# Optimization experiments

Measured on AMD Instinct MI355X. Metric: run time of the kernel, lower is better.

The kernel has to match this reference:

```python
import jax, jax.numpy as jnp
import numpy as np

B, D = 2048, 1024
TEMP = 0.1
LAMBDA_CS_REG = 0.5


def setup_inputs() -> dict:
    key = jax.random.key(0)
    k1, k2, k3, k4, k5 = jax.random.split(key, 5)
    return {
        "english": jax.random.normal(k1, (B, D), dtype=jnp.float32),
        "etok": jax.random.normal(k2, (B, D), dtype=jnp.float32),
        "ktoe": jax.random.normal(k3, (B, D), dtype=jnp.float32),
        "korean": jax.random.normal(k4, (B, D), dtype=jnp.float32),
        "cs_ratios": jax.random.uniform(k5, (B,), dtype=jnp.float32),
    }


def _l2norm(x):
    return x / jnp.linalg.norm(x, axis=1, keepdims=True)


def reference(english, etok, ktoe, korean, cs_ratios):
    e = _l2norm(english)   # [B,D]
    et = _l2norm(etok)
    kt = _l2norm(ktoe)
    k = _l2norm(korean)
    bsz = e.shape[0]

    # Stack the 4 embedding types: order [english, korean, etok, ktoe]
    embs = jnp.stack([e, k, et, kt])           # [4,B,D]

    # Similarities of each anchor row i against every row j of every type t.
    S_e = jnp.einsum("bd,tnd->tbn", e, embs) / TEMP   # [4,B,B] english anchors
    S_k = jnp.einsum("bd,tnd->tbn", k, embs) / TEMP   # [4,B,B] korean anchors
    exp_Se = jnp.exp(S_e)
    exp_Sk = jnp.exp(S_k)

    diag_e = jnp.diagonal(exp_Se, axis1=1, axis2=2)   # [4,B] exp(sim(anchor_i, type_i))
    diag_k = jnp.diagonal(exp_Sk, axis1=1, axis2=2)

    # Negatives: all 4 types for every j != i.
    neg_e = exp_Se.sum(axis=(0, 2)) - diag_e.sum(axis=0)   # [B]
    neg_k = exp_Sk.sum(axis=(0, 2)) - diag_k.sum(axis=0)

    # Positives: eng anchor -> {etok_i, ktoe_i, korean_i}; kor anchor -> {etok_i, ktoe_i, english_i}
    num_e = diag_e[1] + diag_e[2] + diag_e[3]
    num_k = diag_k[0] + diag_k[2] + diag_k[3]

    loss_e = -jnp.log(num_e / (num_e + neg_e))
    loss_k = -jnp.log(num_k / (num_k + neg_k))
    contrastive_loss = (loss_e + loss_k).sum() / (2 * bsz)

    # Code-switch regularization
    r = cs_ratios[:, None]                              # [B,1]
    etok_reg = jnp.linalg.norm(et - (r * e + (1 - r) * k), axis=1)
    ktoe_reg = jnp.linalg.norm(kt - ((1 - r) * e + r * k), axis=1)
    cs_reg_loss = (etok_reg + ktoe_reg).sum() / bsz

    total_loss = contrastive_loss + LAMBDA_CS_REG * cs_reg_loss
    return total_loss, contrastive_loss, cs_reg_loss
```

## Files before the change

kernel.cpp:

```cpp
#include <hip/hip_runtime.h>
#include <hip/hip_bf16.h>
#include <math.h>

#define NB   2048
#define ND   1024
#define INV_TEMP 10.0f
#define LAMBDA_CS 0.5f

using short8  = __attribute__((ext_vector_type(8))) short;
using floatx4 = __attribute__((ext_vector_type(4))) float;

__device__ __forceinline__ ushort f32_to_bf16_rne(float f) {
  union { float f; unsigned u; } v; v.f = f;
  unsigned u = v.u;
  u += 0x7FFFu + ((u >> 16) & 1u);
  return (ushort)(u >> 16);
}

__global__ __launch_bounds__(256) void k_norm_reg(
    const float* __restrict__ e, const float* __restrict__ k,
    const float* __restrict__ et, const float* __restrict__ kt,
    const float* __restrict__ ratios,
    ushort* __restrict__ M, float* __restrict__ reg_partial)
{
  const int b = blockIdx.x, tid = threadIdx.x;
  const int wave = tid >> 6, lane = tid & 63;

  float4 ve  = ((const float4*)(e  + (size_t)b * ND))[tid];
  float4 vk  = ((const float4*)(k  + (size_t)b * ND))[tid];
  float4 vet = ((const float4*)(et + (size_t)b * ND))[tid];
  float4 vkt = ((const float4*)(kt + (size_t)b * ND))[tid];

  float s0 = ve.x*ve.x + ve.y*ve.y + ve.z*ve.z + ve.w*ve.w;
  float s1 = vk.x*vk.x + vk.y*vk.y + vk.z*vk.z + vk.w*vk.w;
  float s2 = vet.x*vet.x + vet.y*vet.y + vet.z*vet.z + vet.w*vet.w;
  float s3 = vkt.x*vkt.x + vkt.y*vkt.y + vkt.z*vkt.z + vkt.w*vkt.w;
  #pragma unroll
  for (int o = 1; o < 64; o <<= 1) {
    s0 += __shfl_xor(s0, o); s1 += __shfl_xor(s1, o);
    s2 += __shfl_xor(s2, o); s3 += __shfl_xor(s3, o);
  }
  __shared__ float red[4][4];
  if (lane == 0) { red[wave][0] = s0; red[wave][1] = s1; red[wave][2] = s2; red[wave][3] = s3; }
  __syncthreads();
  const float ie  = 1.0f / sqrtf(red[0][0] + red[1][0] + red[2][0] + red[3][0]);
  const float ik  = 1.0f / sqrtf(red[0][1] + red[1][1] + red[2][1] + red[3][1]);
  const float iet = 1.0f / sqrtf(red[0][2] + red[1][2] + red[2][2] + red[3][2]);
  const float ikt = 1.0f / sqrtf(red[0][3] + red[1][3] + red[2][3] + red[3][3]);

  {
    ushort o4[4];
    o4[0] = f32_to_bf16_rne(ve.x * ie);  o4[1] = f32_to_bf16_rne(ve.y * ie);
    o4[2] = f32_to_bf16_rne(ve.z * ie);  o4[3] = f32_to_bf16_rne(ve.w * ie);
    *(ushort4*)(M + ((size_t)0 * NB + b) * ND + tid * 4) = *(ushort4*)o4;
    o4[0] = f32_to_bf16_rne(vk.x * ik);  o4[1] = f32_to_bf16_rne(vk.y * ik);
    o4[2] = f32_to_bf16_rne(vk.z * ik);  o4[3] = f32_to_bf16_rne(vk.w * ik);
    *(ushort4*)(M + ((size_t)1 * NB + b) * ND + tid * 4) = *(ushort4*)o4;
    o4[0] = f32_to_bf16_rne(vet.x * iet); o4[1] = f32_to_bf16_rne(vet.y * iet);
    o4[2] = f32_to_bf16_rne(vet.z * iet); o4[3] = f32_to_bf16_rne(vet.w * iet);
    *(ushort4*)(M + ((size_t)2 * NB + b) * ND + tid * 4) = *(ushort4*)o4;
    o4[0] = f32_to_bf16_rne(vkt.x * ikt); o4[1] = f32_to_bf16_rne(vkt.y * ikt);
    o4[2] = f32_to_bf16_rne(vkt.z * ikt); o4[3] = f32_to_bf16_rne(vkt.w * ikt);
    *(ushort4*)(M + ((size_t)3 * NB + b) * ND + tid * 4) = *(ushort4*)o4;
  }

  const float r = ratios[b], rm = 1.0f - r;
  float a1 = 0.f, a2 = 0.f;
  {
    float en, kn, d1, d2;
    en = ve.x*ie; kn = vk.x*ik;
    d1 = vet.x*iet - (r*en + rm*kn); d2 = vkt.x*ikt - (rm*en + r*kn);
    a1 += d1*d1; a2 += d2*d2;
    en = ve.y*ie; kn = vk.y*ik;
    d1 = vet.y*iet - (r*en + rm*kn); d2 = vkt.y*ikt - (rm*en + r*kn);
    a1 += d1*d1; a2 += d2*d2;
    en = ve.z*ie; kn = vk.z*ik;
    d1 = vet.z*iet - (r*en + rm*kn); d2 = vkt.z*ikt - (rm*en + r*kn);
    a1 += d1*d1; a2 += d2*d2;
    en = ve.w*ie; kn = vk.w*ik;
    d1 = vet.w*iet - (r*en + rm*kn); d2 = vkt.w*ikt - (rm*en + r*kn);
    a1 += d1*d1; a2 += d2*d2;
  }
  #pragma unroll
  for (int o = 1; o < 64; o <<= 1) { a1 += __shfl_xor(a1, o); a2 += __shfl_xor(a2, o); }
  __shared__ float red2[4][2];
  if (lane == 0) { red2[wave][0] = a1; red2[wave][1] = a2; }
  __syncthreads();
  if (tid == 0) {
    float t1 = red2[0][0] + red2[1][0] + red2[2][0] + red2[3][0];
    float t2 = red2[0][1] + red2[1][1] + red2[2][1] + red2[3][1];
    reg_partial[b] = sqrtf(t1) + sqrtf(t2);
  }
}

__global__ __launch_bounds__(256) void k_gemm_exp_rowsum(
    const ushort* __restrict__ M,
    float* __restrict__ rsp,
    float* __restrict__ diag)
{
  __shared__ ushort As[128 * 32];
  __shared__ ushort Bs[128 * 32];
  __shared__ float redR[256];
  __shared__ float redC[256];

  int bx, by;
  {
    int idx = blockIdx.x;
    if (idx < 1024) { by = idx >> 5; bx = 32 + (idx & 31); }
    else {
      int t = idx - 1024; by = 0;
      while (t >= 32 - by) { t -= 32 - by; ++by; }
      bx = by + t;
    }
  }
  const bool sym = (bx < 32) && (bx > by);
  const int j0 = bx * 128;
  const int i0 = by * 128;

  const int tid  = threadIdx.x;
  const int wave = tid >> 6;
  const int lane = tid & 63;
  const int q = lane >> 4;
  const int m = lane & 15;
  const int wrow = (wave >> 1) * 64;
  const int wcol = (wave & 1) * 64;

  floatx4 acc[4][4] = {};

  const int srow = lane >> 2;
  const int scol = (lane & 3) ^ ((srow >> 1) & 3);
  const int c0 = wave * 2, c1 = c0 + 1;

  const ushort* gA = M + (size_t)i0 * ND;
  const ushort* gB = M + (size_t)j0 * ND;

  int aoff[4], boff[4];
  #pragma unroll
  for (int x = 0; x < 4; ++x) {
    const int sw = (q ^ ((m >> 1) & 3)) * 8;
    aoff[x] = (wrow + x * 16 + m) * 32 + sw;
    boff[x] = (wcol + x * 16 + m) * 32 + sw;
  }

  for (int k0 = 0; k0 < ND; k0 += 32) {
    __syncthreads();
    {
      const ushort* g = gA + (size_t)(c0 * 16 + srow) * ND + k0 + scol * 8;
      __builtin_amdgcn_global_load_lds(
          (const __attribute__((address_space(1))) unsigned int*)g,
          (__attribute__((address_space(3))) unsigned int*)&As[c0 * 512], 16, 0, 0);
    }
    {
      const ushort* g = gA + (size_t)(c1 * 16 + srow) * ND + k0 + scol * 8;
      __builtin_amdgcn_global_load_lds(
          (const __attribute__((address_space(1))) unsigned int*)g,
          (__attribute__((address_space(3))) unsigned int*)&As[c1 * 512], 16, 0, 0);
    }
    {
      const ushort* g = gB + (size_t)(c0 * 16 + srow) * ND + k0 + scol * 8;
      __builtin_amdgcn_global_load_lds(
          (const __attribute__((address_space(1))) unsigned int*)g,
          (__attribute__((address_space(3))) unsigned int*)&Bs[c0 * 512], 16, 0, 0);
    }
    {
      const ushort* g = gB + (size_t)(c1 * 16 + srow) * ND + k0 + scol * 8;
      __builtin_amdgcn_global_load_lds(
          (const __attribute__((address_space(1))) unsigned int*)g,
          (__attribute__((address_space(3))) unsigned int*)&Bs[c1 * 512], 16, 0, 0);
    }
    __syncthreads();

    short8 af[4], bf[4];
    #pragma unroll
    for (int x = 0; x < 4; ++x) {
      af[x] = *(const short8*)&As[aoff[x]];
      bf[x] = *(const short8*)&Bs[boff[x]];
    }
    #pragma unroll
    for (int mi = 0; mi < 4; ++mi)
      #pragma unroll
      for (int ni = 0; ni < 4; ++ni)
        acc[mi][ni] = __builtin_amdgcn_mfma_f32_16x16x32_bf16(
            af[mi], bf[ni], acc[mi][ni], 0, 0, 0);
  }

  float colAcc[4] = {0.f, 0.f, 0.f, 0.f};
  #pragma unroll
  for (int mi = 0; mi < 4; ++mi) {
    #pragma unroll
    for (int r = 0; r < 4; ++r) {
      const int ig = i0 + wrow + mi * 16 + q * 4 + r;
      float s = 0.f;
      #pragma unroll
      for (int ni = 0; ni < 4; ++ni) {
        float v = __expf(acc[mi][ni][r] * INV_TEMP);
        s += v;
        colAcc[ni] += v;
        const int jg = j0 + wcol + ni * 16 + m;
        if ((jg & (NB - 1)) == (ig & (NB - 1))) {
          diag[(((ig >> 11) << 2) + (jg >> 11)) * NB + (ig & (NB - 1))] = v;
        }
      }
      s += __shfl_xor(s, 1);
      s += __shfl_xor(s, 2);
      s += __shfl_xor(s, 4);
      s += __shfl_xor(s, 8);
      if (m == 0) redR[(wave & 1) * 128 + wrow + mi * 16 + q * 4 + r] = s;
    }
  }
  #pragma unroll
  for (int ni = 0; ni < 4; ++ni) {
    float c = colAcc[ni];
    c += __shfl_xor(c, 16);
    c += __shfl_xor(c, 32);
    if (q == 0) redC[(wave >> 1) * 128 + wcol + ni * 16 + m] = c;
  }
  __syncthreads();
  if (tid < 128) {
    rsp[(size_t)bx * 4096 + i0 + tid] = redR[tid] + redR[128 + tid];
    if (sym)
      rsp[(size_t)by * 4096 + j0 + tid] = redC[tid] + redC[128 + tid];
  }
}

__global__ __launch_bounds__(256) void k_rowloss(
    const float* __restrict__ rsp, const float* __restrict__ diag,
    float* __restrict__ loss_row)
{
  const int n = blockIdx.x * 256 + threadIdx.x;
  float se = 0.f, sk = 0.f;
  #pragma unroll 8
  for (int s = 0; s < 64; ++s) {
    se += rsp[s * 4096 + n];
    sk += rsp[s * 4096 + 2048 + n];
  }
  const float d_ee  = diag[0 * NB + n];
  const float d_ek  = diag[1 * NB + n];
  const float d_eet = diag[2 * NB + n];
  const float d_ekt = diag[3 * NB + n];
  const float d_kk  = diag[5 * NB + n];
  const float d_ket = diag[6 * NB + n];
  const float d_kkt = diag[7 * NB + n];
  const float num_e = d_ek + d_eet + d_ekt;
  const float den_e = se - d_ee;
  const float num_k = d_ek + d_ket + d_kkt;
  const float den_k = sk - d_kk;
  loss_row[n] = logf(den_e / num_e) + logf(den_k / num_k);
}

__global__ __launch_bounds__(256) void k_out(
    const float* __restrict__ loss_row, const float* __restrict__ reg_partial,
    float* __restrict__ out)
{
  const int tid = threadIdx.x;
  const int wave = tid >> 6, lane = tid & 63;
  float l = 0.f, g = 0.f;
  #pragma unroll
  for (int i = 0; i < 8; ++i) {
    l += loss_row[tid + i * 256];
    g += reg_partial[tid + i * 256];
  }
  #pragma unroll
  for (int o = 1; o < 64; o <<= 1) { l += __shfl_xor(l, o); g += __shfl_xor(g, o); }
  __shared__ float rl[4], rg[4];
  if (lane == 0) { rl[wave] = l; rg[wave] = g; }
  __syncthreads();
  if (tid == 0) {
    float contrastive = (rl[0] + rl[1] + rl[2] + rl[3]) * (1.0f / (2.0f * NB));
    float cs = (rg[0] + rg[1] + rg[2] + rg[3]) * (1.0f / NB);
    out[0] = contrastive + LAMBDA_CS * cs;
    out[1] = contrastive;
    out[2] = cs;
  }
}

extern "C" void kernel_launch(void* const* d_in, const int* in_sizes, int n_in,
                              void* d_out, int out_size, void* d_ws, size_t ws_size,
                              hipStream_t stream) {
  const float* english = (const float*)d_in[0];
  const float* etok    = (const float*)d_in[1];
  const float* ktoe    = (const float*)d_in[2];
  const float* korean  = (const float*)d_in[3];
  const float* ratios  = (const float*)d_in[4];

  char* ws = (char*)d_ws;
  const size_t OFF_M    = 0;
  const size_t OFF_RSP  = OFF_M + (size_t)8192 * 1024 * 2;
  const size_t OFF_DIAG = OFF_RSP + (size_t)64 * 4096 * 4;
  const size_t OFF_REG  = OFF_DIAG + 8 * NB * sizeof(float);
  const size_t OFF_LOSS = OFF_REG + NB * sizeof(float);

  ushort* M           = (ushort*)(ws + OFF_M);
  float* rsp          = (float*)(ws + OFF_RSP);
  float* diag         = (float*)(ws + OFF_DIAG);
  float* reg_partial  = (float*)(ws + OFF_REG);
  float* loss_row     = (float*)(ws + OFF_LOSS);

  k_norm_reg<<<dim3(NB), 256, 0, stream>>>(english, korean, etok, ktoe, ratios, M, reg_partial);
  k_gemm_exp_rowsum<<<dim3(1552), 256, 0, stream>>>(M, rsp, diag);
  k_rowloss<<<dim3(8), 256, 0, stream>>>(rsp, diag, loss_row);
  k_out<<<dim3(1), 256, 0, stream>>>(loss_row, reg_partial, (float*)d_out);
}
```

Before: 165.2 us.

## Use 256x256 double-buffered GEMM tiles with phased loads and fused final reduction

Rewrites the similarity GEMM to use 256x256 output tiles with 512 threads, double-buffered LDS with 64-wide K slices, and interleaved global-to-LDS staging across phases with explicit waitcnt/barrier and setprio around the MFMA bursts. This is meant to raise arithmetic intensity and hide load latency compared with the previous single-buffered 128x128 tiles. The row-loss and output kernels are merged into one 1024-thread kernel, removing one launch. The cost is higher register and LDS use (128KB of LDS, 32 accumulators per thread), fewer blocks (392) on the device, and a fragile hand-written pipeline schedule.

```diff
diff --git a/kernel.cpp b/kernel.cpp
--- a/kernel.cpp
+++ b/kernel.cpp
@@ -1,5 +1,4 @@
 #include <hip/hip_runtime.h>
-#include <hip/hip_bf16.h>
 #include <math.h>
 
 #define NB   2048
@@ -93,111 +92,141 @@
   }
 }
 
-__global__ __launch_bounds__(256) void k_gemm_exp_rowsum(
+
+#define STAGE_A(TT, HH, BUF) do {                                              \
+  _Pragma("unroll")                                                            \
+  for (int L_ = 0; L_ < 2; ++L_) {                                             \
+    const int u_ = L_ * 512 + tid;                                             \
+    const int rr_ = u_ >> 3;                                                   \
+    const int sc_ = ((u_ & 7) * 16) ^ ((rr_ & 7) << 4);                        \
+    const ushort* gp_ = M + (size_t)(i0 + (HH)*128 + rr_) * ND + (TT)*64 + (sc_ >> 1); \
+    __builtin_amdgcn_global_load_lds(                                          \
+        (const __attribute__((address_space(1))) unsigned int*)gp_,            \
+        (__attribute__((address_space(3))) unsigned int*)&As[BUF][(HH)*8192 + L_*4096 + wave*512], \
+        16, 0, 0);                                                             \
+  }                                                                            \
+} while (0)
+
+#define STAGE_B(TT, HH, BUF) do {                                              \
+  _Pragma("unroll")                                                            \
+  for (int L_ = 0; L_ < 2; ++L_) {                                             \
+    const int u_ = L_ * 512 + tid;                                             \
+    const int rr_ = u_ >> 3;                                                   \
+    const int sc_ = ((u_ & 7) * 16) ^ ((rr_ & 7) << 4);                        \
+    const ushort* gp_ = M + (size_t)(j0 + (HH)*128 + rr_) * ND + (TT)*64 + (sc_ >> 1); \
+    __builtin_amdgcn_global_load_lds(                                          \
+        (const __attribute__((address_space(1))) unsigned int*)gp_,            \
+        (__attribute__((address_space(3))) unsigned int*)&Bs[BUF][(HH)*8192 + L_*4096 + wave*512], \
+        16, 0, 0);                                                             \
+  }                                                                            \
+} while (0)
+
+#define PHASE(BUF, MQ, KK, LOADB, WAIT, STMT) do {                             \
+  short8 af_[4];                                                               \
+  _Pragma("unroll")                                                            \
+  for (int mi_ = 0; mi_ < 4; ++mi_) {                                          \
+    const int row_ = wrow + ((MQ)*4 + mi_)*16 + m;                             \
+    const int cb_ = ((KK)*64 + q*16) ^ ((row_ & 7) << 4);                      \
+    af_[mi_] = *(const short8*)&As[BUF][row_*64 + (cb_ >> 1)];                 \
+  }                                                                            \
+  if (LOADB) {                                                                 \
+    _Pragma("unroll")                                                          \
+    for (int ni_ = 0; ni_ < 4; ++ni_) {                                        \
+      const int rb_ = wcol + ni_*16 + m;                                       \
+      const int cb_ = ((KK)*64 + q*16) ^ ((rb_ & 7) << 4);                     \
+      bfr[KK][ni_] = *(const short8*)&Bs[BUF][rb_*64 + (cb_ >> 1)];            \
+    }                                                                          \
+  }                                                                            \
+  STMT;                                                                        \
+  __builtin_amdgcn_s_barrier();                                                \
+  asm volatile("s_waitcnt lgkmcnt(0)" ::: "memory");                           \
+  __builtin_amdgcn_s_setprio(1);                                               \
+  _Pragma("unroll")                                                            \
+  for (int mi_ = 0; mi_ < 4; ++mi_)                                            \
+    _Pragma("unroll")                                                          \
+    for (int ni_ = 0; ni_ < 4; ++ni_)                                          \
+      acc[(MQ)*4 + mi_][ni_] = __builtin_amdgcn_mfma_f32_16x16x32_bf16(        \
+          af_[mi_], bfr[KK][ni_], acc[(MQ)*4 + mi_][ni_], 0, 0, 0);            \
+  __builtin_amdgcn_s_setprio(0);                                               \
+  if (WAIT) asm volatile("s_waitcnt vmcnt(4)" ::: "memory");                   \
+  __builtin_amdgcn_s_barrier();                                                \
+} while (0)
+
+__global__ __launch_bounds__(512, 2) void k_gemm_exp_rowsum(
     const ushort* __restrict__ M,
     float* __restrict__ rsp,
     float* __restrict__ diag)
 {
-  __shared__ ushort As[128 * 32];
-  __shared__ ushort Bs[128 * 32];
-  __shared__ float redR[256];
-  __shared__ float redC[256];
+  __shared__ __align__(16) ushort As[2][16384];
+  __shared__ __align__(16) ushort Bs[2][16384];
 
   int bx, by;
   {
     int idx = blockIdx.x;
-    if (idx < 1024) { by = idx >> 5; bx = 32 + (idx & 31); }
+    if (idx < 256) { by = idx >> 4; bx = 16 + (idx & 15); }
     else {
-      int t = idx - 1024; by = 0;
-      while (t >= 32 - by) { t -= 32 - by; ++by; }
+      int t = idx - 256; by = 0;
+      while (t >= 16 - by) { t -= 16 - by; ++by; }
       bx = by + t;
     }
   }
-  const bool sym = (bx < 32) && (bx > by);
-  const int j0 = bx * 128;
-  const int i0 = by * 128;
+  const bool sym = (bx < 16) && (bx > by);
+  const int i0 = by * 256;
+  const int j0 = bx * 256;
 
   const int tid  = threadIdx.x;
   const int wave = tid >> 6;
   const int lane = tid & 63;
   const int q = lane >> 4;
   const int m = lane & 15;
-  const int wrow = (wave >> 1) * 64;
-  const int wcol = (wave & 1) * 64;
-
-  floatx4 acc[4][4] = {};
-
-  const int srow = lane >> 2;
-  const int scol = (lane & 3) ^ ((srow >> 1) & 3);
-  const int c0 = wave * 2, c1 = c0 + 1;
-
-  const ushort* gA = M + (size_t)i0 * ND;
-  const ushort* gB = M + (size_t)j0 * ND;
-
-  int aoff[4], boff[4];
-  #pragma unroll
-  for (int x = 0; x < 4; ++x) {
-    const int sw = (q ^ ((m >> 1) & 3)) * 8;
-    aoff[x] = (wrow + x * 16 + m) * 32 + sw;
-    boff[x] = (wcol + x * 16 + m) * 32 + sw;
-  }
-
-  for (int k0 = 0; k0 < ND; k0 += 32) {
-    __syncthreads();
-    {
-      const ushort* g = gA + (size_t)(c0 * 16 + srow) * ND + k0 + scol * 8;
-      __builtin_amdgcn_global_load_lds(
-          (const __attribute__((address_space(1))) unsigned int*)g,
-          (__attribute__((address_space(3))) unsigned int*)&As[c0 * 512], 16, 0, 0);
-    }
-    {
-      const ushort* g = gA + (size_t)(c1 * 16 + srow) * ND + k0 + scol * 8;
-      __builtin_amdgcn_global_load_lds(
-          (const __attribute__((address_space(1))) unsigned int*)g,
-          (__attribute__((address_space(3))) unsigned int*)&As[c1 * 512], 16, 0, 0);
-    }
-    {
-      const ushort* g = gB + (size_t)(c0 * 16 + srow) * ND + k0 + scol * 8;
-      __builtin_amdgcn_global_load_lds(
-          (const __attribute__((address_space(1))) unsigned int*)g,
-          (__attribute__((address_space(3))) unsigned int*)&Bs[c0 * 512], 16, 0, 0);
-    }
-    {
-      const ushort* g = gB + (size_t)(c1 * 16 + srow) * ND + k0 + scol * 8;
-      __builtin_amdgcn_global_load_lds(
-          (const __attribute__((address_space(1))) unsigned int*)g,
-          (__attribute__((address_space(3))) unsigned int*)&Bs[c1 * 512], 16, 0, 0);
-    }
-    __syncthreads();
-
-    short8 af[4], bf[4];
-    #pragma unroll
-    for (int x = 0; x < 4; ++x) {
-      af[x] = *(const short8*)&As[aoff[x]];
-      bf[x] = *(const short8*)&Bs[boff[x]];
-    }
-    #pragma unroll
-    for (int mi = 0; mi < 4; ++mi)
-      #pragma unroll
-      for (int ni = 0; ni < 4; ++ni)
-        acc[mi][ni] = __builtin_amdgcn_mfma_f32_16x16x32_bf16(
-            af[mi], bf[ni], acc[mi][ni], 0, 0, 0);
-  }
+  const int wr = wave >> 2;
+  const int wc = wave & 3;
+  const int wrow = wr * 128;
+  const int wcol = wc * 64;
+
+  floatx4 acc[8][4] = {};
+  short8 bfr[2][4];
+
+  STAGE_A(0, 0, 0); STAGE_A(0, 1, 0);
+  STAGE_B(0, 0, 0); STAGE_B(0, 1, 0);
+  STAGE_B(1, 0, 1); STAGE_B(1, 1, 1);
+  asm volatile("s_waitcnt vmcnt(4)" ::: "memory");
+  __builtin_amdgcn_s_barrier();
+
+  #pragma unroll 1
+  for (int i = 0; i < 8; ++i) {
+    const int t1 = 2*i + 1;
+    const int t2 = (2*i + 2) & 15;
+    const int t3 = (2*i + 3) & 15;
+    PHASE(0, 0, 0, 1, 0, STAGE_A(t1, 0, 1));
+    PHASE(0, 0, 1, 1, 0, STAGE_A(t1, 1, 1));
+    PHASE(0, 1, 0, 0, 0, STAGE_B(t2, 0, 0));
+    PHASE(0, 1, 1, 0, 1, STAGE_B(t2, 1, 0));
+    PHASE(1, 0, 0, 1, 0, STAGE_A(t2, 0, 0));
+    PHASE(1, 0, 1, 1, 0, STAGE_A(t2, 1, 0));
+    PHASE(1, 1, 0, 0, 0, STAGE_B(t3, 0, 1));
+    PHASE(1, 1, 1, 0, 1, STAGE_B(t3, 1, 1));
+  }
+
+  __syncthreads();
+
+  float* redR = (float*)&As[0][0];
+  float* redC = redR + 1024;
 
   float colAcc[4] = {0.f, 0.f, 0.f, 0.f};
   #pragma unroll
-  for (int mi = 0; mi < 4; ++mi) {
+  for (int mi = 0; mi < 8; ++mi) {
     #pragma unroll
     for (int r = 0; r < 4; ++r) {
       const int ig = i0 + wrow + mi * 16 + q * 4 + r;
       float s = 0.f;
       #pragma unroll
       for (int ni = 0; ni < 4; ++ni) {
-        float v = __expf(acc[mi][ni][r] * INV_TEMP);
+        const float v = __expf(acc[mi][ni][r] * INV_TEMP);
         s += v;
         colAcc[ni] += v;
         const int jg = j0 + wcol + ni * 16 + m;
-        if ((jg & (NB - 1)) == (ig & (NB - 1))) {
+        if (((ig ^ jg) & (NB - 1)) == 0) {
           diag[(((ig >> 11) << 2) + (jg >> 11)) * NB + (ig & (NB - 1))] = v;
         }
       }
@@ -205,7 +234,7 @@
       s += __shfl_xor(s, 2);
       s += __shfl_xor(s, 4);
       s += __shfl_xor(s, 8);
-      if (m == 0) redR[(wave & 1) * 128 + wrow + mi * 16 + q * 4 + r] = s;
+      if (m == 0) redR[wc * 256 + wrow + mi * 16 + q * 4 + r] = s;
     }
   }
   #pragma unroll
@@ -213,61 +242,58 @@
     float c = colAcc[ni];
     c += __shfl_xor(c, 16);
     c += __shfl_xor(c, 32);
-    if (q == 0) redC[(wave >> 1) * 128 + wcol + ni * 16 + m] = c;
-  }
-  __syncthreads();
-  if (tid < 128) {
-    rsp[(size_t)bx * 4096 + i0 + tid] = redR[tid] + redR[128 + tid];
-    if (sym)
-      rsp[(size_t)by * 4096 + j0 + tid] = redC[tid] + redC[128 + tid];
-  }
-}
-
-__global__ __launch_bounds__(256) void k_rowloss(
+    if (q == 0) redC[wr * 256 + wcol + ni * 16 + m] = c;
+  }
+  __syncthreads();
+  if (tid < 256) {
+    const float rs = redR[tid] + redR[256 + tid] + redR[512 + tid] + redR[768 + tid];
+    rsp[(size_t)bx * 4096 + i0 + tid] = rs;
+    if (sym) {
+      const float cs = redC[tid] + redC[256 + tid];
+      rsp[(size_t)by * 4096 + j0 + tid] = cs;
+    }
+  }
+}
+
+__global__ __launch_bounds__(1024) void k_final(
     const float* __restrict__ rsp, const float* __restrict__ diag,
-    float* __restrict__ loss_row)
-{
-  const int n = blockIdx.x * 256 + threadIdx.x;
-  float se = 0.f, sk = 0.f;
-  #pragma unroll 8
-  for (int s = 0; s < 64; ++s) {
-    se += rsp[s * 4096 + n];
-    sk += rsp[s * 4096 + 2048 + n];
-  }
-  const float d_ee  = diag[0 * NB + n];
-  const float d_ek  = diag[1 * NB + n];
-  const float d_eet = diag[2 * NB + n];
-  const float d_ekt = diag[3 * NB + n];
-  const float d_kk  = diag[5 * NB + n];
-  const float d_ket = diag[6 * NB + n];
-  const float d_kkt = diag[7 * NB + n];
-  const float num_e = d_ek + d_eet + d_ekt;
-  const float den_e = se - d_ee;
-  const float num_k = d_ek + d_ket + d_kkt;
-  const float den_k = sk - d_kk;
-  loss_row[n] = logf(den_e / num_e) + logf(den_k / num_k);
-}
-
-__global__ __launch_bounds__(256) void k_out(
-    const float* __restrict__ loss_row, const float* __restrict__ reg_partial,
-    float* __restrict__ out)
+    const float* __restrict__ reg_partial, float* __restrict__ out)
 {
   const int tid = threadIdx.x;
   const int wave = tid >> 6, lane = tid & 63;
   float l = 0.f, g = 0.f;
   #pragma unroll
-  for (int i = 0; i < 8; ++i) {
-    l += loss_row[tid + i * 256];
-    g += reg_partial[tid + i * 256];
+  for (int h = 0; h < 2; ++h) {
+    const int n = tid + h * 1024;
+    float se = 0.f, sk = 0.f;
+    #pragma unroll 8
+    for (int s = 0; s < 32; ++s) {
+      se += rsp[s * 4096 + n];
+      sk += rsp[s * 4096 + 2048 + n];
+    }
+    const float d_ee  = diag[0 * NB + n];
+    const float d_ek  = diag[1 * NB + n];
+    const float d_eet = diag[2 * NB + n];
+    const float d_ekt = diag[3 * NB + n];
+    const float d_kk  = diag[5 * NB + n];
+    const float d_ket = diag[6 * NB + n];
+    const float d_kkt = diag[7 * NB + n];
+    const float num_e = d_ek + d_eet + d_ekt;
+    const float num_k = d_ek + d_ket + d_kkt;
+    l += logf((se - d_ee) / num_e) + logf((sk - d_kk) / num_k);
+    g += reg_partial[n];
   }
   #pragma unroll
   for (int o = 1; o < 64; o <<= 1) { l += __shfl_xor(l, o); g += __shfl_xor(g, o); }
-  __shared__ float rl[4], rg[4];
+  __shared__ float rl[16], rg[16];
   if (lane == 0) { rl[wave] = l; rg[wave] = g; }
   __syncthreads();
   if (tid == 0) {
-    float contrastive = (rl[0] + rl[1] + rl[2] + rl[3]) * (1.0f / (2.0f * NB));
-    float cs = (rg[0] + rg[1] + rg[2] + rg[3]) * (1.0f / NB);
+    float L = 0.f, G = 0.f;
+    #pragma unroll
+    for (int i = 0; i < 16; ++i) { L += rl[i]; G += rg[i]; }
+    const float contrastive = L * (1.0f / (2.0f * NB));
+    const float cs = G * (1.0f / NB);
     out[0] = contrastive + LAMBDA_CS * cs;
     out[1] = contrastive;
     out[2] = cs;
@@ -286,18 +312,15 @@
   char* ws = (char*)d_ws;
   const size_t OFF_M    = 0;
   const size_t OFF_RSP  = OFF_M + (size_t)8192 * 1024 * 2;
-  const size_t OFF_DIAG = OFF_RSP + (size_t)64 * 4096 * 4;
+  const size_t OFF_DIAG = OFF_RSP + (size_t)32 * 4096 * 4;
   const size_t OFF_REG  = OFF_DIAG + 8 * NB * sizeof(float);
-  const size_t OFF_LOSS = OFF_REG + NB * sizeof(float);
 
   ushort* M           = (ushort*)(ws + OFF_M);
   float* rsp          = (float*)(ws + OFF_RSP);
   float* diag         = (float*)(ws + OFF_DIAG);
   float* reg_partial  = (float*)(ws + OFF_REG);
-  float* loss_row     = (float*)(ws + OFF_LOSS);
 
   k_norm_reg<<<dim3(NB), 256, 0, stream>>>(english, korean, etok, ktoe, ratios, M, reg_partial);
-  k_gemm_exp_rowsum<<<dim3(1552), 256, 0, stream>>>(M, rsp, diag);
-  k_rowloss<<<dim3(8), 256, 0, stream>>>(rsp, diag, loss_row);
-  k_out<<<dim3(1), 256, 0, stream>>>(loss_row, reg_partial, (float*)d_out);
-}
+  k_gemm_exp_rowsum<<<dim3(392), 512, 0, stream>>>(M, rsp, diag);
+  k_final<<<dim3(1), 1024, 0, stream>>>(rsp, diag, reg_partial, (float*)d_out);
+}
```

Result: slower. 171.9 us (+4.0%).

## Triple-buffer GEMM LDS loads and replace partial rowsum buffers with atomics

Applied to the files above, without the earlier changes.

The GEMM main loop now prefetches K-tiles two steps ahead into a three-stage LDS ring, using explicit vmcnt waits and a single barrier per step. This is meant to hide global-load latency behind the MFMA work, at the cost of three times the LDS per block. Row sums are now accumulated with atomicAdd into a single 4096-entry buffer that the norm kernel zeroes, replacing the 64-way partial array. The rowloss and output kernels are merged into one 1024-thread kernel, which removes one launch and the partial-sum traffic.

```diff
diff --git a/kernel.cpp b/kernel.cpp
--- a/kernel.cpp
+++ b/kernel.cpp
@@ -1,5 +1,4 @@
 #include <hip/hip_runtime.h>
-#include <hip/hip_bf16.h>
 #include <math.h>
 
 #define NB   2048
@@ -21,7 +20,8 @@
     const float* __restrict__ e, const float* __restrict__ k,
     const float* __restrict__ et, const float* __restrict__ kt,
     const float* __restrict__ ratios,
-    ushort* __restrict__ M, float* __restrict__ reg_partial)
+    ushort* __restrict__ M, float* __restrict__ reg_partial,
+    float* __restrict__ rowsum)
 {
   const int b = blockIdx.x, tid = threadIdx.x;
   const int wave = tid >> 6, lane = tid & 63;
@@ -90,16 +90,35 @@
     float t1 = red2[0][0] + red2[1][0] + red2[2][0] + red2[3][0];
     float t2 = red2[0][1] + red2[1][1] + red2[2][1] + red2[3][1];
     reg_partial[b] = sqrtf(t1) + sqrtf(t2);
-  }
-}
-
-__global__ __launch_bounds__(256) void k_gemm_exp_rowsum(
+    rowsum[b] = 0.f;
+    rowsum[NB + b] = 0.f;
+  }
+}
+
+
+#define GLDS(GP, LP)                                                           \
+  __builtin_amdgcn_global_load_lds(                                            \
+      (const __attribute__((address_space(1))) unsigned int*)(GP),             \
+      (__attribute__((address_space(3))) unsigned int*)(LP), 16, 0, 0)
+
+#define STAGE(TT, BUF) do {                                                    \
+  GLDS(gA + (size_t)(c0 * 16 + srow) * ND + (TT) * 32 + scol * 8,              \
+       &As[BUF][c0 * 512]);                                                    \
+  GLDS(gA + (size_t)(c1 * 16 + srow) * ND + (TT) * 32 + scol * 8,              \
+       &As[BUF][c1 * 512]);                                                    \
+  GLDS(gB + (size_t)(c0 * 16 + srow) * ND + (TT) * 32 + scol * 8,              \
+       &Bs[BUF][c0 * 512]);                                                    \
+  GLDS(gB + (size_t)(c1 * 16 + srow) * ND + (TT) * 32 + scol * 8,              \
+       &Bs[BUF][c1 * 512]);                                                    \
+} while (0)
+
+__global__ __launch_bounds__(256, 3) void k_gemm_exp_rowsum(
     const ushort* __restrict__ M,
-    float* __restrict__ rsp,
+    float* __restrict__ rowsum,
     float* __restrict__ diag)
 {
-  __shared__ ushort As[128 * 32];
-  __shared__ ushort Bs[128 * 32];
+  __shared__ __align__(16) ushort As[3][4096];
+  __shared__ __align__(16) ushort Bs[3][4096];
   __shared__ float redR[256];
   __shared__ float redC[256];
 
@@ -142,47 +161,41 @@
     boff[x] = (wcol + x * 16 + m) * 32 + sw;
   }
 
-  for (int k0 = 0; k0 < ND; k0 += 32) {
-    __syncthreads();
-    {
-      const ushort* g = gA + (size_t)(c0 * 16 + srow) * ND + k0 + scol * 8;
-      __builtin_amdgcn_global_load_lds(
-          (const __attribute__((address_space(1))) unsigned int*)g,
-          (__attribute__((address_space(3))) unsigned int*)&As[c0 * 512], 16, 0, 0);
-    }
-    {
-      const ushort* g = gA + (size_t)(c1 * 16 + srow) * ND + k0 + scol * 8;
-      __builtin_amdgcn_global_load_lds(
-          (const __attribute__((address_space(1))) unsigned int*)g,
-          (__attribute__((address_space(3))) unsigned int*)&As[c1 * 512], 16, 0, 0);
-    }
-    {
-      const ushort* g = gB + (size_t)(c0 * 16 + srow) * ND + k0 + scol * 8;
-      __builtin_amdgcn_global_load_lds(
-          (const __attribute__((address_space(1))) unsigned int*)g,
-          (__attribute__((address_space(3))) unsigned int*)&Bs[c0 * 512], 16, 0, 0);
-    }
-    {
-      const ushort* g = gB + (size_t)(c1 * 16 + srow) * ND + k0 + scol * 8;
-      __builtin_amdgcn_global_load_lds(
-          (const __attribute__((address_space(1))) unsigned int*)g,
-          (__attribute__((address_space(3))) unsigned int*)&Bs[c1 * 512], 16, 0, 0);
-    }
-    __syncthreads();
+  STAGE(0, 0);
+  STAGE(1, 1);
+  asm volatile("s_waitcnt vmcnt(4)" ::: "memory");
+  __builtin_amdgcn_s_barrier();
+
+  int bcur = 0, bnext = 1, bstage = 2;
+  #pragma unroll 1
+  for (int t = 0; t < 32; ++t) {
+    STAGE((t + 2) & 31, bstage);
 
     short8 af[4], bf[4];
     #pragma unroll
     for (int x = 0; x < 4; ++x) {
-      af[x] = *(const short8*)&As[aoff[x]];
-      bf[x] = *(const short8*)&Bs[boff[x]];
+      af[x] = *(const short8*)&As[bcur][aoff[x]];
+      bf[x] = *(const short8*)&Bs[bcur][boff[x]];
     }
+    asm volatile("s_waitcnt lgkmcnt(0)" ::: "memory");
+    __builtin_amdgcn_sched_barrier(0);
+
+    __builtin_amdgcn_s_setprio(1);
     #pragma unroll
     for (int mi = 0; mi < 4; ++mi)
       #pragma unroll
       for (int ni = 0; ni < 4; ++ni)
         acc[mi][ni] = __builtin_amdgcn_mfma_f32_16x16x32_bf16(
             af[mi], bf[ni], acc[mi][ni], 0, 0, 0);
-  }
+    __builtin_amdgcn_s_setprio(0);
+
+    asm volatile("s_waitcnt vmcnt(4)" ::: "memory");
+    __builtin_amdgcn_s_barrier();
+
+    const int tmp = bcur; bcur = bnext; bnext = bstage; bstage = tmp;
+  }
+
+  __syncthreads();
 
   float colAcc[4] = {0.f, 0.f, 0.f, 0.f};
   #pragma unroll
@@ -193,11 +206,11 @@
       float s = 0.f;
       #pragma unroll
       for (int ni = 0; ni < 4; ++ni) {
-        float v = __expf(acc[mi][ni][r] * INV_TEMP);
+        const float v = __expf(acc[mi][ni][r] * INV_TEMP);
         s += v;
         colAcc[ni] += v;
         const int jg = j0 + wcol + ni * 16 + m;
-        if ((jg & (NB - 1)) == (ig & (NB - 1))) {
+        if (((ig ^ jg) & (NB - 1)) == 0) {
           diag[(((ig >> 11) << 2) + (jg >> 11)) * NB + (ig & (NB - 1))] = v;
         }
       }
@@ -217,57 +230,47 @@
   }
   __syncthreads();
   if (tid < 128) {
-    rsp[(size_t)bx * 4096 + i0 + tid] = redR[tid] + redR[128 + tid];
+    atomicAdd(&rowsum[i0 + tid], redR[tid] + redR[128 + tid]);
     if (sym)
-      rsp[(size_t)by * 4096 + j0 + tid] = redC[tid] + redC[128 + tid];
-  }
-}
-
-__global__ __launch_bounds__(256) void k_rowloss(
-    const float* __restrict__ rsp, const float* __restrict__ diag,
-    float* __restrict__ loss_row)
-{
-  const int n = blockIdx.x * 256 + threadIdx.x;
-  float se = 0.f, sk = 0.f;
-  #pragma unroll 8
-  for (int s = 0; s < 64; ++s) {
-    se += rsp[s * 4096 + n];
-    sk += rsp[s * 4096 + 2048 + n];
-  }
-  const float d_ee  = diag[0 * NB + n];
-  const float d_ek  = diag[1 * NB + n];
-  const float d_eet = diag[2 * NB + n];
-  const float d_ekt = diag[3 * NB + n];
-  const float d_kk  = diag[5 * NB + n];
-  const float d_ket = diag[6 * NB + n];
-  const float d_kkt = diag[7 * NB + n];
-  const float num_e = d_ek + d_eet + d_ekt;
-  const float den_e = se - d_ee;
-  const float num_k = d_ek + d_ket + d_kkt;
-  const float den_k = sk - d_kk;
-  loss_row[n] = logf(den_e / num_e) + logf(den_k / num_k);
-}
-
-__global__ __launch_bounds__(256) void k_out(
-    const float* __restrict__ loss_row, const float* __restrict__ reg_partial,
-    float* __restrict__ out)
+      atomicAdd(&rowsum[j0 + tid], redC[tid] + redC[128 + tid]);
+  }
+}
+
+__global__ __launch_bounds__(1024) void k_final(
+    const float* __restrict__ rowsum, const float* __restrict__ diag,
+    const float* __restrict__ reg_partial, float* __restrict__ out)
 {
   const int tid = threadIdx.x;
   const int wave = tid >> 6, lane = tid & 63;
   float l = 0.f, g = 0.f;
   #pragma unroll
-  for (int i = 0; i < 8; ++i) {
-    l += loss_row[tid + i * 256];
-    g += reg_partial[tid + i * 256];
+  for (int h = 0; h < 2; ++h) {
+    const int n = tid + h * 1024;
+    const float se = rowsum[n];
+    const float sk = rowsum[NB + n];
+    const float d_ee  = diag[0 * NB + n];
+    const float d_ek  = diag[1 * NB + n];
+    const float d_eet = diag[2 * NB + n];
+    const float d_ekt = diag[3 * NB + n];
+    const float d_kk  = diag[5 * NB + n];
+    const float d_ket = diag[6 * NB + n];
+    const float d_kkt = diag[7 * NB + n];
+    const float num_e = d_ek + d_eet + d_ekt;
+    const float num_k = d_ek + d_ket + d_kkt;
+    l += logf((se - d_ee) / num_e) + logf((sk - d_kk) / num_k);
+    g += reg_partial[n];
   }
   #pragma unroll
   for (int o = 1; o < 64; o <<= 1) { l += __shfl_xor(l, o); g += __shfl_xor(g, o); }
-  __shared__ float rl[4], rg[4];
+  __shared__ float rl[16], rg[16];
   if (lane == 0) { rl[wave] = l; rg[wave] = g; }
   __syncthreads();
   if (tid == 0) {
-    float contrastive = (rl[0] + rl[1] + rl[2] + rl[3]) * (1.0f / (2.0f * NB));
-    float cs = (rg[0] + rg[1] + rg[2] + rg[3]) * (1.0f / NB);
+    float L = 0.f, G = 0.f;
+    #pragma unroll
+    for (int i = 0; i < 16; ++i) { L += rl[i]; G += rg[i]; }
+    const float contrastive = L * (1.0f / (2.0f * NB));
+    const float cs = G * (1.0f / NB);
     out[0] = contrastive + LAMBDA_CS * cs;
     out[1] = contrastive;
     out[2] = cs;
@@ -285,19 +288,16 @@
 
   char* ws = (char*)d_ws;
   const size_t OFF_M    = 0;
-  const size_t OFF_RSP  = OFF_M + (size_t)8192 * 1024 * 2;
-  const size_t OFF_DIAG = OFF_RSP + (size_t)64 * 4096 * 4;
+  const size_t OFF_ROW  = OFF_M + (size_t)8192 * 1024 * 2;
+  const size_t OFF_DIAG = OFF_ROW + (size_t)4096 * 4;
   const size_t OFF_REG  = OFF_DIAG + 8 * NB * sizeof(float);
-  const size_t OFF_LOSS = OFF_REG + NB * sizeof(float);
 
   ushort* M           = (ushort*)(ws + OFF_M);
-  float* rsp          = (float*)(ws + OFF_RSP);
+  float* rowsum       = (float*)(ws + OFF_ROW);
   float* diag         = (float*)(ws + OFF_DIAG);
   float* reg_partial  = (float*)(ws + OFF_REG);
-  float* loss_row     = (float*)(ws + OFF_LOSS);
-
-  k_norm_reg<<<dim3(NB), 256, 0, stream>>>(english, korean, etok, ktoe, ratios, M, reg_partial);
-  k_gemm_exp_rowsum<<<dim3(1552), 256, 0, stream>>>(M, rsp, diag);
-  k_rowloss<<<dim3(8), 256, 0, stream>>>(rsp, diag, loss_row);
-  k_out<<<dim3(1), 256, 0, stream>>>(loss_row, reg_partial, (float*)d_out);
-}
+
+  k_norm_reg<<<dim3(NB), 256, 0, stream>>>(english, korean, etok, ktoe, ratios, M, reg_partial, rowsum);
+  k_gemm_exp_rowsum<<<dim3(1552), 256, 0, stream>>>(M, rowsum, diag);
+  k_final<<<dim3(1), 1024, 0, stream>>>(rowsum, diag, reg_partial, (float*)d_out);
+}
```

Measured after the change: 168.1 us. No clear change (+1.8%).
